# Kernel optimization log

Hardware: AMD Instinct MI355X
Metric: run time of the kernel (lower is better)

## Reference

```python
import jax, jax.numpy as jnp
import numpy as np
import math

B, HID, T, D = 4, 1024, 2048, 1024
NEG_INF = -2.0**15 + 1.0  # matches torch constant -32767.0


def setup_inputs() -> dict:
    key = jax.random.key(0)
    ks = jax.random.split(key, 9)
    s = 0.02
    return {
        "minibatch": jax.random.normal(ks[0], (B, HID, T), dtype=jnp.float32),
        "emb_w": jax.random.normal(ks[1], (D, HID), dtype=jnp.float32) * s,
        "emb_b": jax.random.normal(ks[2], (D,), dtype=jnp.float32) * s,
        "key_w": jax.random.normal(ks[3], (D, D), dtype=jnp.float32) * s,
        "key_b": jax.random.normal(ks[4], (D,), dtype=jnp.float32) * s,
        "query_w": jax.random.normal(ks[5], (D, D), dtype=jnp.float32) * s,
        "query_b": jax.random.normal(ks[6], (D,), dtype=jnp.float32) * s,
        "value_w": jax.random.normal(ks[7], (D, D), dtype=jnp.float32) * s,
        "value_b": jax.random.normal(ks[8], (D,), dtype=jnp.float32) * s,
    }


def reference(minibatch, emb_w, emb_b, key_w, key_b, query_w, query_b, value_w, value_b):
    # minibatch: [B, hidden, T] -> permute -> [B, T, hidden]
    x = jnp.transpose(minibatch, (0, 2, 1))
    m = x @ emb_w.T + emb_b                      # [B, T, D]
    keys = m @ key_w.T + key_b                   # [B, T, D]
    queries = m @ query_w.T + query_b            # [B, T, D]
    values = m @ value_w.T + value_b             # [B, T, D]
    logits = jnp.einsum('btd,bsd->bts', queries, keys)  # [B, T, T]
    mask = jnp.tril(jnp.ones((logits.shape[1], logits.shape[2]), dtype=bool))
    logits = jnp.where(mask[None], logits, jnp.float32(NEG_INF))
    # NOTE: original code applies softmax over dim=1 (query axis) and divides
    # by sqrt(d_model) AFTER the softmax — reproduced faithfully here.
    probs = jax.nn.softmax(logits, axis=1) / jnp.float32(math.sqrt(D))
    read = jnp.einsum('bts,bsd->btd', probs, values)     # [B, T, D]
    out = read + m
    return jnp.transpose(out, (0, 2, 1))                  # [B, D, T]
```

## Files before the change

kernel.cpp:

```cpp
#include <hip/hip_runtime.h>

#define T_DIM 2048
#define D_DIM 1024
#define H_DIM 1024
#define B_DIM 4

typedef __attribute__((ext_vector_type(8))) __bf16 bf16x8;
typedef __attribute__((ext_vector_type(4))) float f32x4;

__device__ __forceinline__ unsigned short f2b(float f) {
  union { float f; unsigned int u; } x; x.f = f;
  unsigned int r = x.u + 0x7fffu + ((x.u >> 16) & 1u);
  return (unsigned short)(r >> 16);
}
__device__ __forceinline__ float b2f(unsigned short b) {
  union { unsigned int u; float f; } x; x.u = ((unsigned int)b) << 16;
  return x.f;
}

__device__ __forceinline__ void async16(unsigned short* l, const unsigned short* g) {
  __builtin_amdgcn_global_load_lds((const __attribute__((address_space(1))) void*)g,
                                   (__attribute__((address_space(3))) void*)l,
                                   16, 0, 0);
}

__global__ __launch_bounds__(256) void prep_kernel(const float* __restrict__ ew,
                                                   const float* __restrict__ kw,
                                                   const float* __restrict__ qw,
                                                   const float* __restrict__ vw,
                                                   const float* __restrict__ kb,
                                                   const float* __restrict__ qb,
                                                   const float* __restrict__ vb,
                                                   unsigned short* __restrict__ oe,
                                                   unsigned short* __restrict__ okqv,
                                                   float* __restrict__ ob) {
  int bid = blockIdx.x;
  if (bid == 4096) {
    #pragma unroll
    for (int k = 0; k < 3; k++) {
      int f4 = threadIdx.x + k * 256;
      int fi = f4 * 4;
      const float* src = fi < 1024 ? kb + fi : (fi < 2048 ? qb + (fi - 1024) : vb + (fi - 2048));
      *(float4*)(&ob[fi]) = *(const float4*)src;
    }
    return;
  }
  int i = bid * 256 + threadIdx.x;
  int seg = i >> 18;
  int off = i & 262143;
  const float* in = seg == 0 ? ew : (seg == 1 ? kw : (seg == 2 ? qw : vw));
  unsigned short* out = seg == 0 ? oe : okqv + (size_t)(seg - 1) * 1048576;
  float4 v = ((const float4*)in)[off];
  ushort4 o;
  o.x = f2b(v.x); o.y = f2b(v.y); o.z = f2b(v.z); o.w = f2b(v.w);
  ((ushort4*)out)[off] = o;
}

template <typename TIN>
__global__ __launch_bounds__(256) void transpose_kernel(const TIN* __restrict__ in,
                                                        unsigned short* __restrict__ out,
                                                        int inLD, size_t sIn, int R, size_t sOut) {
  __shared__ TIN tile[32][33];
  int c0 = blockIdx.x * 32, r0 = blockIdx.y * 32;
  int tx = threadIdx.x & 31, ty = threadIdx.x >> 5;
  const TIN* I = in + (size_t)blockIdx.z * sIn;
  #pragma unroll
  for (int i = 0; i < 32; i += 8)
    tile[ty + i][tx] = I[(size_t)(r0 + ty + i) * inLD + (c0 + tx)];
  __syncthreads();
  unsigned short* O = out + (size_t)blockIdx.z * sOut;
  #pragma unroll
  for (int i = 0; i < 32; i += 8) {
    TIN v = tile[tx][ty + i];
    unsigned short bb;
    if constexpr (sizeof(TIN) == 4) bb = f2b((float)v);
    else bb = (unsigned short)v;
    O[(size_t)(c0 + ty + i) * R + (r0 + tx)] = bb;
  }
}


#define BAR_ asm volatile("s_barrier" ::: "memory")
#define VM6_ asm volatile("s_waitcnt vmcnt(6)" ::: "memory")
#define VM0_ asm volatile("s_waitcnt vmcnt(0)" ::: "memory")

#define STGA3(t, bb, u) async16(smem + (bb) * 24576 + (u) * 4096 + tid * 8, \
                                A + (size_t)((u) * 64 + rl0) * lda + (t) * 64 + ce)
#define STGB3(t, bb, u) async16(smem + (bb) * 24576 + 8192 + (u) * 4096 + tid * 8, \
                                Bm + (size_t)((u) * 64 + rl0) * ldb + (t) * 64 + ce)
#define STGTILE(t, bb) do { STGA3(t, bb, 0); STGA3(t, bb, 1); \
    STGB3(t, bb, 0); STGB3(t, bb, 1); STGB3(t, bb, 2); STGB3(t, bb, 3); } while (0)

#define FRG(base, row, ks) \
  (*(const bf16x8*)((base) + (row) * 64 + ((((ks) << 2) | hi) ^ (lo & 7)) * 8))

#define LOADFRAGS(bA, bB)                                            \
  _Pragma("unroll") for (int m_ = 0; m_ < 4; m_++) {                 \
    af[m_][0] = FRG(bA, wr * 64 + m_ * 16 + lo, 0);                  \
    af[m_][1] = FRG(bA, wr * 64 + m_ * 16 + lo, 1);                  \
  }                                                                  \
  _Pragma("unroll") for (int n_ = 0; n_ < 4; n_++) {                 \
    bg[n_][0] = FRG(bB, wc * 64 + n_ * 16 + lo, 0);                  \
    bg[n_][1] = FRG(bB, wc * 64 + n_ * 16 + lo, 1);                  \
  }

#define MFMA32_                                                          \
  __builtin_amdgcn_s_setprio(1);                                         \
  _Pragma("unroll") for (int ks_ = 0; ks_ < 2; ks_++)                    \
    _Pragma("unroll") for (int m_ = 0; m_ < 4; m_++)                     \
      _Pragma("unroll") for (int n_ = 0; n_ < 4; n_++)                   \
        acc[m_][n_] = __builtin_amdgcn_mfma_f32_16x16x32_bf16(           \
            af[m_][ks_], bg[n_][ks_], acc[m_][n_], 0, 0, 0);             \
  __builtin_amdgcn_s_setprio(0);

template <int OMODE, bool BIAS, int SKIP>
__global__ __launch_bounds__(512, 2)
void gemm8_kernel(const unsigned short* __restrict__ A,
                  const unsigned short* __restrict__ Bm,
                  const float* __restrict__ bias,
                  float* __restrict__ Cf, unsigned short* __restrict__ Cb,
                  const unsigned short* __restrict__ mres,
                  int N, int K, int lda, int ldb,
                  size_t sAb, size_t sBb, size_t sCb) {
  __shared__ __align__(16) unsigned short smem[73728];

  int gx = gridDim.x;
  int nwg = gx * gridDim.y;
  int flat = blockIdx.x + gx * blockIdx.y;
  int cpx = nwg >> 3;
  int f2 = (flat & 7) * cpx + (flat >> 3);
  int bn = f2 % gx, bm = f2 / gx;
  int bz = blockIdx.z;
  if (SKIP == 1 && bn * 2 + 1 < bm) return;

  A  += (size_t)bz * sAb + (size_t)bm * 128 * lda;
  Bm += (size_t)bz * sBb + (size_t)bn * 256 * ldb;

  int tid = threadIdx.x;
  int lane = tid & 63, wid = tid >> 6;
  int wr = wid >> 2, wc = wid & 3;
  int lo = lane & 15, hi = lane >> 4;
  int rl0 = tid >> 3;
  int ce = 8 * ((tid & 7) ^ (rl0 & 7));

  int nt = K / 64;
  if (SKIP == 2) nt = (bm + 1) * 2;

  bf16x8 af[4][2], bg[4][2];
  f32x4 acc[4][4] = {};

  STGTILE(0, 0);
  STGTILE(1, 1);
  VM6_; BAR_;

  int cur = 0;
  for (int t = 0; t < nt - 2; t++) {
    const unsigned short* bA = smem + cur * 24576;
    const unsigned short* bB = bA + 8192;
    LOADFRAGS(bA, bB)
    int b2 = cur + 2; if (b2 >= 3) b2 -= 3;
    STGTILE(t + 2, b2);
    MFMA32_
    VM6_; BAR_;
    cur = (cur + 1 == 3) ? 0 : cur + 1;
  }
  {
    const unsigned short* bA = smem + cur * 24576;
    const unsigned short* bB = bA + 8192;
    LOADFRAGS(bA, bB)
    MFMA32_
    VM0_; BAR_;
    cur = (cur + 1 == 3) ? 0 : cur + 1;
  }
  {
    const unsigned short* bA = smem + cur * 24576;
    const unsigned short* bB = bA + 8192;
    LOADFRAGS(bA, bB)
    MFMA32_
  }

  __syncthreads();
  int row0 = bm * 128, col0 = bn * 256;
  size_t coff = (size_t)bz * sCb;

  if (OMODE == 1) {
    unsigned short* ep = smem;
    #pragma unroll
    for (int n = 0; n < 4; n++) {
      int cl = wc * 64 + n * 16 + lo;
      float bv = BIAS ? bias[col0 + cl] : 0.f;
      #pragma unroll
      for (int m = 0; m < 4; m++) {
        int rl = wr * 64 + m * 16 + hi * 4;
        #pragma unroll
        for (int j = 0; j < 4; j++)
          ep[(rl + j) * 264 + cl] = f2b(acc[m][n][j] + bv);
      }
    }
    __syncthreads();
    #pragma unroll
    for (int it = 0; it < 8; it++) {
      int idx = it * 512 + tid, r = idx >> 5, c = idx & 31;
      *(uint4*)(Cb + coff + (size_t)(row0 + r) * N + col0 + c * 8) =
          *(const uint4*)(ep + r * 264 + c * 8);
    }
  } else if (OMODE == 2) {
    float* ep = (float*)smem;
    #pragma unroll
    for (int half = 0; half < 2; half++) {
      __syncthreads();
      if (wr == half) {
        #pragma unroll
        for (int n = 0; n < 4; n++) {
          int cl = wc * 64 + n * 16 + lo;
          #pragma unroll
          for (int m = 0; m < 4; m++) {
            int rl = m * 16 + hi * 4;
            #pragma unroll
            for (int j = 0; j < 4; j++) ep[(rl + j) * 260 + cl] = acc[m][n][j];
          }
        }
      }
      __syncthreads();
      #pragma unroll
      for (int it = 0; it < 8; it++) {
        int idx = it * 512 + tid, r = idx >> 6, c = idx & 63;
        *(float4*)(Cf + coff + (size_t)(row0 + half * 64 + r) * N + col0 + c * 4) =
            *(const float4*)(ep + r * 260 + c * 4);
      }
    }
  } else {
    float* ep = (float*)smem;
    #pragma unroll
    for (int half = 0; half < 2; half++) {
      __syncthreads();
      if ((wc >> 1) == half) {
        #pragma unroll
        for (int n = 0; n < 4; n++) {
          int cl = wc * 64 + n * 16 + lo;
          #pragma unroll
          for (int m = 0; m < 4; m++) {
            int rl = wr * 64 + m * 16 + hi * 4;
            #pragma unroll
            for (int j = 0; j < 4; j++) {
              float v = acc[m][n][j] +
                        b2f(mres[((size_t)bz * T_DIM + row0 + rl + j) * D_DIM + col0 + cl]);
              ep[(cl & 127) * 132 + rl + j] = v;
            }
          }
        }
      }
      __syncthreads();
      #pragma unroll
      for (int it = 0; it < 8; it++) {
        int idx = it * 512 + tid, r = idx >> 5, c = idx & 31;
        *(float4*)(Cf + ((size_t)bz * D_DIM + col0 + half * 128 + r) * T_DIM + row0 + c * 4) =
            *(const float4*)(ep + r * 132 + c * 4);
      }
    }
  }
}

__device__ __forceinline__ float wred_max(float v) {
  #pragma unroll
  for (int o = 32; o > 0; o >>= 1) v = fmaxf(v, __shfl_down(v, o, 64));
  return v;
}
__device__ __forceinline__ float wred_sum(float v) {
  #pragma unroll
  for (int o = 32; o > 0; o >>= 1) v += __shfl_down(v, o, 64);
  return v;
}

__global__ __launch_bounds__(256) void softmax_stats_kernel(const float* __restrict__ lg,
                                                            float* __restrict__ smax,
                                                            float* __restrict__ sinv) {
  __shared__ float sb[4];
  int row = blockIdx.x;
  int s = row & (T_DIM - 1);
  int t0 = (s >> 8) << 8;
  const float* Lr = lg + (size_t)row * T_DIM;
  float mx = -3.4e38f;
  for (int t = t0 + threadIdx.x; t < T_DIM; t += 256)
    if (t >= s) mx = fmaxf(mx, Lr[t]);
  mx = wred_max(mx);
  if ((threadIdx.x & 63) == 0) sb[threadIdx.x >> 6] = mx;
  __syncthreads();
  mx = fmaxf(fmaxf(sb[0], sb[1]), fmaxf(sb[2], sb[3]));
  __syncthreads();
  float sum = 0.f;
  for (int t = t0 + threadIdx.x; t < T_DIM; t += 256)
    if (t >= s) sum += __expf(Lr[t] - mx);
  sum = wred_sum(sum);
  if ((threadIdx.x & 63) == 0) sb[threadIdx.x >> 6] = sum;
  __syncthreads();
  if (threadIdx.x == 0) {
    float tot = sb[0] + sb[1] + sb[2] + sb[3];
    smax[row] = mx;
    sinv[row] = 1.0f / (tot * 32.0f);
  }
}

__global__ __launch_bounds__(256) void probs_kernel(const float* __restrict__ lg,
                                                    const float* __restrict__ smax,
                                                    const float* __restrict__ sinv,
                                                    unsigned short* __restrict__ probs) {
  int bz = blockIdx.z;
  int t0 = blockIdx.x * 32, s0 = blockIdx.y * 32;
  if (s0 >= (((t0 >> 7) + 1) << 7)) return;
  __shared__ float tile[32][33];
  int tx = threadIdx.x & 31, ty = threadIdx.x >> 5;
  const float* L = lg + (size_t)bz * T_DIM * T_DIM;
  #pragma unroll
  for (int i = 0; i < 32; i += 8)
    tile[ty + i][tx] = L[(size_t)(s0 + ty + i) * T_DIM + (t0 + tx)];
  __syncthreads();
  unsigned short* P = probs + (size_t)bz * T_DIM * T_DIM;
  #pragma unroll
  for (int i = 0; i < 32; i += 8) {
    int t = t0 + ty + i, s = s0 + tx;
    float x = tile[tx][ty + i];
    float p = (t >= s) ? __expf(x - smax[bz * T_DIM + s]) * sinv[bz * T_DIM + s] : 0.f;
    P[(size_t)t * T_DIM + s] = f2b(p);
  }
}

extern "C" void kernel_launch(void* const* d_in, const int* in_sizes, int n_in,
                              void* d_out, int out_size, void* d_ws, size_t ws_size,
                              hipStream_t stream) {
  const float* minibatch = (const float*)d_in[0];
  const float* emb_w   = (const float*)d_in[1];
  const float* emb_b   = (const float*)d_in[2];
  const float* key_w   = (const float*)d_in[3];
  const float* key_b   = (const float*)d_in[4];
  const float* query_w = (const float*)d_in[5];
  const float* query_b = (const float*)d_in[6];
  const float* value_w = (const float*)d_in[7];
  const float* value_b = (const float*)d_in[8];
  float* out = (float*)d_out;

  char* ws = (char*)d_ws;
  const size_t MB = 1ull << 20;
  unsigned short* wbf_emb = (unsigned short*)(ws + 0 * MB);
  unsigned short* wbf_kqv = (unsigned short*)(ws + 2 * MB);
  float*          kqv_b   = (float*)(ws + 8 * MB);
  unsigned short* m_bf    = (unsigned short*)(ws + 9 * MB);
  unsigned short* KQV     = (unsigned short*)(ws + 25 * MB);
  unsigned short* VT_bf   = (unsigned short*)(ws + 73 * MB);
  float*          logitsT = (float*)(ws + 89 * MB);
  unsigned short* xT      = (unsigned short*)(ws + 153 * MB);
  unsigned short* probs   = (unsigned short*)(ws + 153 * MB);
  float*          smax    = (float*)(ws + 186 * MB);
  float*          sinv    = (float*)(ws + 186 * MB + 32768);

  const int BT = B_DIM * T_DIM;
  const size_t TT = (size_t)T_DIM * T_DIM;

  prep_kernel<<<4097, 256, 0, stream>>>(emb_w, key_w, query_w, value_w,
                                        key_b, query_b, value_b,
                                        wbf_emb, wbf_kqv, kqv_b);

  transpose_kernel<float><<<dim3(T_DIM / 32, H_DIM / 32, B_DIM), 256, 0, stream>>>(
      minibatch, xT, T_DIM, (size_t)H_DIM * T_DIM, H_DIM, (size_t)T_DIM * H_DIM);

  gemm8_kernel<1, true, 0><<<dim3(D_DIM / 256, BT / 128, 1), 512, 0, stream>>>(
      xT, wbf_emb, emb_b, nullptr, m_bf, nullptr, D_DIM, H_DIM, H_DIM, H_DIM, 0, 0, 0);

  gemm8_kernel<1, true, 0><<<dim3(3072 / 256, BT / 128, 1), 512, 0, stream>>>(
      m_bf, wbf_kqv, kqv_b, nullptr, KQV, nullptr, 3072, D_DIM, D_DIM, D_DIM, 0, 0, 0);

  transpose_kernel<unsigned short><<<dim3(D_DIM / 32, T_DIM / 32, B_DIM), 256, 0, stream>>>(
      KQV + 2048, VT_bf, 3072, (size_t)T_DIM * 3072, T_DIM, (size_t)D_DIM * T_DIM);

  gemm8_kernel<2, false, 1><<<dim3(T_DIM / 256, T_DIM / 128, B_DIM), 512, 0, stream>>>(
      KQV, KQV + 1024, nullptr, logitsT, nullptr, nullptr, T_DIM, D_DIM, 3072, 3072,
      (size_t)T_DIM * 3072, (size_t)T_DIM * 3072, TT);

  softmax_stats_kernel<<<BT, 256, 0, stream>>>(logitsT, smax, sinv);

  probs_kernel<<<dim3(T_DIM / 32, T_DIM / 32, B_DIM), 256, 0, stream>>>(
      logitsT, smax, sinv, probs);

  gemm8_kernel<4, false, 2><<<dim3(D_DIM / 256, T_DIM / 128, B_DIM), 512, 0, stream>>>(
      probs, VT_bf, nullptr, out, nullptr, m_bf, D_DIM, T_DIM, T_DIM, T_DIM,
      TT, (size_t)D_DIM * T_DIM, 0);
}
```

Baseline: 225.3 us.

## Enlarge GEMM tile to 256x256 with double-buffered, interleaved 8-wave pipeline

Doubles the M tile of the shared bf16 GEMM kernel from 128 to 256 rows, giving each wave a 128x64 output block (acc[8][4]). The LDS plan changes from a triple buffer to a double buffer with separate A/B regions. The K loop is rescheduled into finer phases that interleave fragment loads, async global-to-LDS staging and MFMA blocks between barriers. Causal skipping, probs masking granularity and launch grids are adjusted to match. The aim is more data reuse per loaded byte and better overlap, at the cost of higher register pressure, more barriers, fewer workgroups and coarser causal skipping.

Result: slower. 265.2 us (+17.7%).

```diff
diff --git a/kernel.cpp b/kernel.cpp
--- a/kernel.cpp
+++ b/kernel.cpp
@@ -80,37 +80,46 @@
 }
 
 
-#define BAR_ asm volatile("s_barrier" ::: "memory")
-#define VM6_ asm volatile("s_waitcnt vmcnt(6)" ::: "memory")
-#define VM0_ asm volatile("s_waitcnt vmcnt(0)" ::: "memory")
-
-#define STGA3(t, bb, u) async16(smem + (bb) * 24576 + (u) * 4096 + tid * 8, \
-                                A + (size_t)((u) * 64 + rl0) * lda + (t) * 64 + ce)
-#define STGB3(t, bb, u) async16(smem + (bb) * 24576 + 8192 + (u) * 4096 + tid * 8, \
-                                Bm + (size_t)((u) * 64 + rl0) * ldb + (t) * 64 + ce)
-#define STGTILE(t, bb) do { STGA3(t, bb, 0); STGA3(t, bb, 1); \
-    STGB3(t, bb, 0); STGB3(t, bb, 1); STGB3(t, bb, 2); STGB3(t, bb, 3); } while (0)
+#define BAR_  asm volatile("s_barrier" ::: "memory")
+#define VM8_  asm volatile("s_waitcnt vmcnt(8)" ::: "memory")
+#define VM6_  asm volatile("s_waitcnt vmcnt(6)" ::: "memory")
+#define VM0_  asm volatile("s_waitcnt vmcnt(0)" ::: "memory")
+
+#define STGAH(t, h) do { \
+    unsigned short* d_ = ldsA + ((t) & 1) * 16384 + (h) * 8192 + tid * 8;            \
+    const unsigned short* s_ = A + (size_t)((h) * 128 + rl0) * lda + (t) * 64 + ce;  \
+    async16(d_, s_); async16(d_ + 4096, s_ + (size_t)64 * lda); } while (0)
+#define STGBH(t, h) do { \
+    unsigned short* d_ = ldsB + ((t) & 1) * 16384 + (h) * 8192 + tid * 8;            \
+    const unsigned short* s_ = Bm + (size_t)((h) * 128 + rl0) * ldb + (t) * 64 + ce; \
+    async16(d_, s_); async16(d_ + 4096, s_ + (size_t)64 * ldb); } while (0)
 
 #define FRG(base, row, ks) \
   (*(const bf16x8*)((base) + (row) * 64 + ((((ks) << 2) | hi) ^ (lo & 7)) * 8))
 
-#define LOADFRAGS(bA, bB)                                            \
-  _Pragma("unroll") for (int m_ = 0; m_ < 4; m_++) {                 \
-    af[m_][0] = FRG(bA, wr * 64 + m_ * 16 + lo, 0);                  \
-    af[m_][1] = FRG(bA, wr * 64 + m_ * 16 + lo, 1);                  \
-  }                                                                  \
-  _Pragma("unroll") for (int n_ = 0; n_ < 4; n_++) {                 \
-    bg[n_][0] = FRG(bB, wc * 64 + n_ * 16 + lo, 0);                  \
-    bg[n_][1] = FRG(bB, wc * 64 + n_ * 16 + lo, 1);                  \
-  }
-
-#define MFMA32_                                                          \
-  __builtin_amdgcn_s_setprio(1);                                         \
-  _Pragma("unroll") for (int ks_ = 0; ks_ < 2; ks_++)                    \
-    _Pragma("unroll") for (int m_ = 0; m_ < 4; m_++)                     \
-      _Pragma("unroll") for (int n_ = 0; n_ < 4; n_++)                   \
-        acc[m_][n_] = __builtin_amdgcn_mfma_f32_16x16x32_bf16(           \
-            af[m_][ks_], bg[n_][ks_], acc[m_][n_], 0, 0, 0);             \
+#define LDA_(bA, mb)                                                   \
+  _Pragma("unroll") for (int m_ = 0; m_ < 4; m_++) {                   \
+    int row_ = wr * 128 + ((mb) + m_) * 16 + lo;                       \
+    af[m_][0] = FRG(bA, row_, 0);                                      \
+    af[m_][1] = FRG(bA, row_, 1);                                      \
+  }
+
+#define LDB_(bB, nb, bg)                                               \
+  _Pragma("unroll") for (int n_ = 0; n_ < 2; n_++) {                   \
+    int row_ = wc * 64 + ((nb) + n_) * 16 + lo;                        \
+    bg[n_][0] = FRG(bB, row_, 0);                                      \
+    bg[n_][1] = FRG(bB, row_, 1);                                      \
+  }
+
+#define MM_(mb, nb, bg)                                                              \
+  __builtin_amdgcn_s_setprio(1);                                                     \
+  _Pragma("unroll") for (int m_ = 0; m_ < 4; m_++)                                   \
+    _Pragma("unroll") for (int n_ = 0; n_ < 2; n_++) {                               \
+      acc[(mb) + m_][(nb) + n_] = __builtin_amdgcn_mfma_f32_16x16x32_bf16(           \
+          af[m_][0], bg[n_][0], acc[(mb) + m_][(nb) + n_], 0, 0, 0);                 \
+      acc[(mb) + m_][(nb) + n_] = __builtin_amdgcn_mfma_f32_16x16x32_bf16(           \
+          af[m_][1], bg[n_][1], acc[(mb) + m_][(nb) + n_], 0, 0, 0);                 \
+    }                                                                                \
   __builtin_amdgcn_s_setprio(0);
 
 template <int OMODE, bool BIAS, int SKIP>
@@ -122,7 +131,9 @@
                   const unsigned short* __restrict__ mres,
                   int N, int K, int lda, int ldb,
                   size_t sAb, size_t sBb, size_t sCb) {
-  __shared__ __align__(16) unsigned short smem[73728];
+  __shared__ __align__(16) unsigned short smem[65536];
+  unsigned short* ldsA = smem;
+  unsigned short* ldsB = smem + 32768;
 
   int gx = gridDim.x;
   int nwg = gx * gridDim.y;
@@ -131,9 +142,9 @@
   int f2 = (flat & 7) * cpx + (flat >> 3);
   int bn = f2 % gx, bm = f2 / gx;
   int bz = blockIdx.z;
-  if (SKIP == 1 && bn * 2 + 1 < bm) return;
-
-  A  += (size_t)bz * sAb + (size_t)bm * 128 * lda;
+  if (SKIP == 1 && bn < bm) return;
+
+  A  += (size_t)bz * sAb + (size_t)bm * 256 * lda;
   Bm += (size_t)bz * sBb + (size_t)bn * 256 * ldb;
 
   int tid = threadIdx.x;
@@ -144,80 +155,95 @@
   int ce = 8 * ((tid & 7) ^ (rl0 & 7));
 
   int nt = K / 64;
-  if (SKIP == 2) nt = (bm + 1) * 2;
-
-  bf16x8 af[4][2], bg[4][2];
-  f32x4 acc[4][4] = {};
-
-  STGTILE(0, 0);
-  STGTILE(1, 1);
-  VM6_; BAR_;
-
-  int cur = 0;
-  for (int t = 0; t < nt - 2; t++) {
-    const unsigned short* bA = smem + cur * 24576;
-    const unsigned short* bB = bA + 8192;
-    LOADFRAGS(bA, bB)
-    int b2 = cur + 2; if (b2 >= 3) b2 -= 3;
-    STGTILE(t + 2, b2);
-    MFMA32_
-    VM6_; BAR_;
-    cur = (cur + 1 == 3) ? 0 : cur + 1;
-  }
-  {
-    const unsigned short* bA = smem + cur * 24576;
-    const unsigned short* bB = bA + 8192;
-    LOADFRAGS(bA, bB)
-    MFMA32_
-    VM0_; BAR_;
-    cur = (cur + 1 == 3) ? 0 : cur + 1;
-  }
-  {
-    const unsigned short* bA = smem + cur * 24576;
-    const unsigned short* bB = bA + 8192;
-    LOADFRAGS(bA, bB)
-    MFMA32_
-  }
-
-  __syncthreads();
-  int row0 = bm * 128, col0 = bn * 256;
+  if (SKIP == 2) nt = (bm + 1) * 4;
+
+  bf16x8 af[4][2], bg0[2][2], bg1[2][2];
+  f32x4 acc[8][4] = {};
+
+  STGAH(0, 0); STGAH(0, 1); STGBH(0, 0); STGBH(0, 1);
+  STGAH(1, 0); STGAH(1, 1); STGBH(1, 0); STGBH(1, 1);
+  VM8_; BAR_;
+
+  const unsigned short* bA0 = ldsA;
+  const unsigned short* bB0 = ldsB;
+  const unsigned short* bA1 = ldsA + 16384;
+  const unsigned short* bB1 = ldsB + 16384;
+
+  int nIter = nt >> 1;
+  for (int i = 0; i < nIter; i++) {
+    bool last = (i == nIter - 1);
+    int ta = 2 * i, tb = ta + 1;
+    LDA_(bA0, 0) LDB_(bB0, 0, bg0)
+    BAR_; MM_(0, 0, bg0) BAR_;
+    LDB_(bB0, 2, bg1)
+    BAR_; MM_(0, 2, bg1) BAR_;
+    LDA_(bA0, 4)
+    if (!last) STGBH(ta + 2, 0);
+    BAR_; MM_(4, 0, bg0) BAR_;
+    if (!last) { STGAH(ta + 2, 0); STGBH(ta + 2, 1); }
+    BAR_; MM_(4, 2, bg1)
+    if (last) { VM0_; } else { VM6_; }
+    BAR_;
+    LDA_(bA1, 0) LDB_(bB1, 0, bg0)
+    if (!last) STGAH(ta + 2, 1);
+    BAR_; MM_(0, 0, bg0) BAR_;
+    LDB_(bB1, 2, bg1)
+    BAR_; MM_(0, 2, bg1) BAR_;
+    LDA_(bA1, 4)
+    if (!last) STGBH(tb + 2, 0);
+    BAR_; MM_(4, 0, bg0) BAR_;
+    if (!last) { STGAH(tb + 2, 0); STGBH(tb + 2, 1); STGAH(tb + 2, 1); }
+    BAR_; MM_(4, 2, bg1)
+    if (!last) VM8_;
+    BAR_;
+  }
+
+  __syncthreads();
+  int row0 = bm * 256, col0 = bn * 256;
   size_t coff = (size_t)bz * sCb;
 
   if (OMODE == 1) {
     unsigned short* ep = smem;
     #pragma unroll
-    for (int n = 0; n < 4; n++) {
-      int cl = wc * 64 + n * 16 + lo;
-      float bv = BIAS ? bias[col0 + cl] : 0.f;
+    for (int half = 0; half < 2; half++) {
+      __syncthreads();
+      if (wr == half) {
+        #pragma unroll
+        for (int n = 0; n < 4; n++) {
+          int cl = wc * 64 + n * 16 + lo;
+          float bv = BIAS ? bias[col0 + cl] : 0.f;
+          #pragma unroll
+          for (int m = 0; m < 8; m++) {
+            int rl = m * 16 + hi * 4;
+            #pragma unroll
+            for (int j = 0; j < 4; j++)
+              ep[(rl + j) * 264 + cl] = f2b(acc[m][n][j] + bv);
+          }
+        }
+      }
+      __syncthreads();
       #pragma unroll
-      for (int m = 0; m < 4; m++) {
-        int rl = wr * 64 + m * 16 + hi * 4;
-        #pragma unroll
-        for (int j = 0; j < 4; j++)
-          ep[(rl + j) * 264 + cl] = f2b(acc[m][n][j] + bv);
-      }
-    }
-    __syncthreads();
-    #pragma unroll
-    for (int it = 0; it < 8; it++) {
-      int idx = it * 512 + tid, r = idx >> 5, c = idx & 31;
-      *(uint4*)(Cb + coff + (size_t)(row0 + r) * N + col0 + c * 8) =
-          *(const uint4*)(ep + r * 264 + c * 8);
+      for (int it = 0; it < 8; it++) {
+        int idx = it * 512 + tid, r = idx >> 5, c = idx & 31;
+        *(uint4*)(Cb + coff + (size_t)(row0 + half * 128 + r) * N + col0 + c * 8) =
+            *(const uint4*)(ep + r * 264 + c * 8);
+      }
     }
   } else if (OMODE == 2) {
     float* ep = (float*)smem;
     #pragma unroll
-    for (int half = 0; half < 2; half++) {
-      __syncthreads();
-      if (wr == half) {
+    for (int q = 0; q < 4; q++) {
+      __syncthreads();
+      if (wr == (q >> 1)) {
+        int mb = (q & 1) * 4;
         #pragma unroll
         for (int n = 0; n < 4; n++) {
           int cl = wc * 64 + n * 16 + lo;
           #pragma unroll
-          for (int m = 0; m < 4; m++) {
-            int rl = m * 16 + hi * 4;
+          for (int mm = 0; mm < 4; mm++) {
+            int rl = mm * 16 + hi * 4;
             #pragma unroll
-            for (int j = 0; j < 4; j++) ep[(rl + j) * 260 + cl] = acc[m][n][j];
+            for (int j = 0; j < 4; j++) ep[(rl + j) * 260 + cl] = acc[mb + mm][n][j];
           }
         }
       }
@@ -225,27 +251,27 @@
       #pragma unroll
       for (int it = 0; it < 8; it++) {
         int idx = it * 512 + tid, r = idx >> 6, c = idx & 63;
-        *(float4*)(Cf + coff + (size_t)(row0 + half * 64 + r) * N + col0 + c * 4) =
+        *(float4*)(Cf + coff + (size_t)(row0 + q * 64 + r) * N + col0 + c * 4) =
             *(const float4*)(ep + r * 260 + c * 4);
       }
     }
   } else {
     float* ep = (float*)smem;
     #pragma unroll
-    for (int half = 0; half < 2; half++) {
-      __syncthreads();
-      if ((wc >> 1) == half) {
+    for (int q = 0; q < 4; q++) {
+      __syncthreads();
+      if (wc == q) {
         #pragma unroll
         for (int n = 0; n < 4; n++) {
-          int cl = wc * 64 + n * 16 + lo;
+          int dl = n * 16 + lo;
           #pragma unroll
-          for (int m = 0; m < 4; m++) {
-            int rl = wr * 64 + m * 16 + hi * 4;
+          for (int m = 0; m < 8; m++) {
+            int rl = wr * 128 + m * 16 + hi * 4;
             #pragma unroll
             for (int j = 0; j < 4; j++) {
               float v = acc[m][n][j] +
-                        b2f(mres[((size_t)bz * T_DIM + row0 + rl + j) * D_DIM + col0 + cl]);
-              ep[(cl & 127) * 132 + rl + j] = v;
+                  b2f(mres[((size_t)bz * T_DIM + row0 + rl + j) * D_DIM + col0 + q * 64 + dl]);
+              ep[dl * 260 + rl + j] = v;
             }
           }
         }
@@ -253,9 +279,9 @@
       __syncthreads();
       #pragma unroll
       for (int it = 0; it < 8; it++) {
-        int idx = it * 512 + tid, r = idx >> 5, c = idx & 31;
-        *(float4*)(Cf + ((size_t)bz * D_DIM + col0 + half * 128 + r) * T_DIM + row0 + c * 4) =
-            *(const float4*)(ep + r * 132 + c * 4);
+        int idx = it * 512 + tid, r = idx >> 6, c = idx & 63;
+        *(float4*)(Cf + ((size_t)bz * D_DIM + col0 + q * 64 + r) * T_DIM + row0 + c * 4) =
+            *(const float4*)(ep + r * 260 + c * 4);
       }
     }
   }
@@ -307,7 +333,7 @@
                                                     unsigned short* __restrict__ probs) {
   int bz = blockIdx.z;
   int t0 = blockIdx.x * 32, s0 = blockIdx.y * 32;
-  if (s0 >= (((t0 >> 7) + 1) << 7)) return;
+  if (s0 >= (((t0 >> 8) + 1) << 8)) return;
   __shared__ float tile[32][33];
   int tx = threadIdx.x & 31, ty = threadIdx.x >> 5;
   const float* L = lg + (size_t)bz * T_DIM * T_DIM;
@@ -363,16 +389,16 @@
   transpose_kernel<float><<<dim3(T_DIM / 32, H_DIM / 32, B_DIM), 256, 0, stream>>>(
       minibatch, xT, T_DIM, (size_t)H_DIM * T_DIM, H_DIM, (size_t)T_DIM * H_DIM);
 
-  gemm8_kernel<1, true, 0><<<dim3(D_DIM / 256, BT / 128, 1), 512, 0, stream>>>(
+  gemm8_kernel<1, true, 0><<<dim3(D_DIM / 256, BT / 256, 1), 512, 0, stream>>>(
       xT, wbf_emb, emb_b, nullptr, m_bf, nullptr, D_DIM, H_DIM, H_DIM, H_DIM, 0, 0, 0);
 
-  gemm8_kernel<1, true, 0><<<dim3(3072 / 256, BT / 128, 1), 512, 0, stream>>>(
+  gemm8_kernel<1, true, 0><<<dim3(3072 / 256, BT / 256, 1), 512, 0, stream>>>(
       m_bf, wbf_kqv, kqv_b, nullptr, KQV, nullptr, 3072, D_DIM, D_DIM, D_DIM, 0, 0, 0);
 
   transpose_kernel<unsigned short><<<dim3(D_DIM / 32, T_DIM / 32, B_DIM), 256, 0, stream>>>(
       KQV + 2048, VT_bf, 3072, (size_t)T_DIM * 3072, T_DIM, (size_t)D_DIM * T_DIM);
 
-  gemm8_kernel<2, false, 1><<<dim3(T_DIM / 256, T_DIM / 128, B_DIM), 512, 0, stream>>>(
+  gemm8_kernel<2, false, 1><<<dim3(T_DIM / 256, T_DIM / 256, B_DIM), 512, 0, stream>>>(
       KQV, KQV + 1024, nullptr, logitsT, nullptr, nullptr, T_DIM, D_DIM, 3072, 3072,
       (size_t)T_DIM * 3072, (size_t)T_DIM * 3072, TT);
 
@@ -381,7 +407,7 @@
   probs_kernel<<<dim3(T_DIM / 32, T_DIM / 32, B_DIM), 256, 0, stream>>>(
       logitsT, smax, sinv, probs);
 
-  gemm8_kernel<4, false, 2><<<dim3(D_DIM / 256, T_DIM / 128, B_DIM), 512, 0, stream>>>(
+  gemm8_kernel<4, false, 2><<<dim3(D_DIM / 256, T_DIM / 256, B_DIM), 512, 0, stream>>>(
       probs, VT_bf, nullptr, out, nullptr, m_bf, D_DIM, T_DIM, T_DIM, T_DIM,
       TT, (size_t)D_DIM * T_DIM, 0);
 }
```
